# Performance work log

Measured on AMD Instinct MI355X. Metric: run time of the kernel, lower is better.

The kernel has to match this reference:

```python
import jax, jax.numpy as jnp
import numpy as np
import math

N_HEADS = 16
ROPE_THETA = 10000.0


def _rope_cos_sin(seqlen, head_dim, theta=ROPE_THETA):
    # freqs_cis = polar(1, outer(t, 1/theta^(2i/d))) -> return cos, sin parts
    inv = 1.0 / (theta ** (jnp.arange(0, head_dim, 2, dtype=jnp.float32) / head_dim))
    t = jnp.arange(seqlen, dtype=jnp.float32)
    freqs = t[:, None] * inv[None, :]          # [S, hd/2]
    return jnp.cos(freqs), jnp.sin(freqs)


def _apply_rope(x, cos, sin):
    # x: [B, S, H, hd]; treat consecutive pairs as complex, rotate by e^{i*freq}
    B, S, H, hd = x.shape
    x2 = x.astype(jnp.float32).reshape(B, S, H, hd // 2, 2)
    xr, xi = x2[..., 0], x2[..., 1]
    c = cos[None, :, None, :]
    s = sin[None, :, None, :]
    out_r = xr * c - xi * s
    out_i = xr * s + xi * c
    return jnp.stack([out_r, out_i], axis=-1).reshape(B, S, H, hd).astype(x.dtype)


def setup_inputs() -> dict:
    key = jax.random.key(0)
    ks = jax.random.split(key, 5)
    dim = 2048
    B, S = 2, 2048
    scale = 1.0 / math.sqrt(dim)
    x = jax.random.normal(ks[0], (B, S, dim), dtype=jnp.float32)
    wq = jax.random.normal(ks[1], (dim, dim), dtype=jnp.float32) * scale
    wk = jax.random.normal(ks[2], (dim, dim), dtype=jnp.float32) * scale
    wv = jax.random.normal(ks[3], (dim, dim), dtype=jnp.float32) * scale
    wo = jax.random.normal(ks[4], (dim, dim), dtype=jnp.float32) * scale
    return {"x": x, "wq": wq, "wk": wk, "wv": wv, "wo": wo}


def reference(x, wq, wk, wv, wo):
    B, S, D = x.shape
    H = N_HEADS
    hd = D // H
    # nn.Linear(bias=False): y = x @ W.T
    q = (x @ wq.T).reshape(B, S, H, hd)
    k = (x @ wk.T).reshape(B, S, H, hd)
    v = (x @ wv.T).reshape(B, S, H, hd)
    cos, sin = _rope_cos_sin(S, hd)
    q = _apply_rope(q, cos, sin)
    k = _apply_rope(k, cos, sin)
    attn = jnp.einsum('bthd,bThd->bhtT', q, k) / jnp.sqrt(jnp.float32(hd))
    attn = jax.nn.softmax(attn, axis=-1)
    out = jnp.einsum('bhtT,bThd->bthd', attn, v).reshape(B, S, D)
    return out @ wo.T
```

## Files before the change

### kernel.cpp

```cpp
#include <hip/hip_runtime.h>
#include <math.h>

typedef unsigned short u16;
typedef __bf16 bf16x8 __attribute__((ext_vector_type(8)));
typedef short s16x4 __attribute__((ext_vector_type(4)));
typedef short s16x8 __attribute__((ext_vector_type(8)));
typedef float f32x4 __attribute__((ext_vector_type(4)));

#define B_ 2
#define S_ 2048
#define D_ 2048
#define H_ 16
#define HD_ 128
#define M_ 4096
#define N3_ 6144

#define AS1(p) ((__attribute__((address_space(1))) void*)(void*)(p))
#define AS3(p) ((__attribute__((address_space(3))) void*)(p))
#define GLD16(g, l) __builtin_amdgcn_global_load_lds(AS1(g), AS3(l), 16, 0, 0)

__device__ __forceinline__ u16 f2bf(float f) {
  unsigned u = __float_as_uint(f);
  return (u16)((u + 0x7FFFu + ((u >> 16) & 1u)) >> 16);
}
__device__ __forceinline__ float bf2f(u16 v) {
  return __uint_as_float(((unsigned)v) << 16);
}

__global__ void cvt_k(const float* __restrict__ src, u16* __restrict__ dst, int n4) {
  int i = blockIdx.x * 256 + threadIdx.x;
  if (i >= n4) return;
  float4 v = ((const float4*)src)[i];
  ushort4 o;
  o.x = f2bf(v.x); o.y = f2bf(v.y); o.z = f2bf(v.z); o.w = f2bf(v.w);
  ((ushort4*)dst)[i] = o;
}

__global__ void rope_tab_k(float2* __restrict__ tab) {
  int t = blockIdx.x * 256 + threadIdx.x;
  if (t >= S_ * 64) return;
  int s = t >> 6, i = t & 63;
  double inv = exp2(-(double)i * (13.287712379549449 / 64.0));
  double fr = (double)s * inv;
  double sv, cv;
  sincos(fr, &sv, &cv);
  tab[t] = make_float2((float)cv, (float)sv);
}

template <typename OT>
__global__ __launch_bounds__(256) void gemm_bt_k(const u16* __restrict__ A,
                                                 const u16* __restrict__ B,
                                                 OT* __restrict__ C,
                                                 int M, int N, int K) {
  __shared__ alignas(16) u16 As[128 * 32];
  __shared__ alignas(16) u16 Bs[128 * 32];
  const int tid = threadIdx.x;
  const int wave = tid >> 6, lane = tid & 63;
  const int quad = lane >> 4, l16 = lane & 15;
  const int m0 = blockIdx.y * 128, n0 = blockIdx.x * 128;
  const int wm = (wave >> 1) * 64, wn = (wave & 1) * 64;
  const u16* Ag = A + (size_t)m0 * K;
  const u16* Bg = B + (size_t)n0 * K;
  f32x4 acc[4][4] = {};
  const int c0 = tid, c1 = tid + 256;
  const int r0 = c0 >> 2, k0b = (c0 & 3) * 8;
  const int r1 = c1 >> 2, k1b = (c1 & 3) * 8;
  u16* la0 = As + (size_t)(wave * 64) * 8;
  u16* la1 = As + (size_t)(256 + wave * 64) * 8;
  u16* lb0 = Bs + (size_t)(wave * 64) * 8;
  u16* lb1 = Bs + (size_t)(256 + wave * 64) * 8;
  for (int kt = 0; kt < K; kt += 32) {
    GLD16(Ag + (size_t)r0 * K + kt + k0b, la0);
    GLD16(Ag + (size_t)r1 * K + kt + k1b, la1);
    GLD16(Bg + (size_t)r0 * K + kt + k0b, lb0);
    GLD16(Bg + (size_t)r1 * K + kt + k1b, lb1);
    __syncthreads();
    bf16x8 af[4], bfr[4];
#pragma unroll
    for (int i = 0; i < 4; ++i)
      af[i] = *(const bf16x8*)&As[(wm + i * 16 + l16) * 32 + quad * 8];
#pragma unroll
    for (int j = 0; j < 4; ++j)
      bfr[j] = *(const bf16x8*)&Bs[(wn + j * 16 + l16) * 32 + quad * 8];
#pragma unroll
    for (int i = 0; i < 4; ++i)
#pragma unroll
      for (int j = 0; j < 4; ++j)
        acc[i][j] = __builtin_amdgcn_mfma_f32_16x16x32_bf16(af[i], bfr[j], acc[i][j], 0, 0, 0);
    __syncthreads();
  }
#pragma unroll
  for (int i = 0; i < 4; ++i) {
#pragma unroll
    for (int j = 0; j < 4; ++j) {
      int n = n0 + wn + j * 16 + l16;
#pragma unroll
      for (int r = 0; r < 4; ++r) {
        int m = m0 + wm + i * 16 + quad * 4 + r;
        if constexpr (sizeof(OT) == 4)
          C[(size_t)m * N + n] = acc[i][j][r];
        else
          C[(size_t)m * N + n] = f2bf(acc[i][j][r]);
      }
    }
  }
}

__global__ void rope_k(const u16* __restrict__ qkv, const float2* __restrict__ tab,
                       u16* __restrict__ Qr, u16* __restrict__ Kr) {
  int t = blockIdx.x * 256 + threadIdx.x;
  int m = t >> 10;
  int h = (t >> 6) & 15;
  int i = t & 63;
  int s = m & (S_ - 1);
  int b = m >> 11;
  float2 cs = tab[(s << 6) | i];
  const u16* qp = qkv + (size_t)m * N3_ + h * HD_ + 2 * i;
  ushort2 qv = *(const ushort2*)qp;
  ushort2 kv = *(const ushort2*)(qp + D_);
  float qr = bf2f(qv.x), qi = bf2f(qv.y);
  float kr = bf2f(kv.x), ki = bf2f(kv.y);
  ushort2 qo, ko;
  qo.x = f2bf(qr * cs.x - qi * cs.y);
  qo.y = f2bf(qr * cs.y + qi * cs.x);
  ko.x = f2bf(kr * cs.x - ki * cs.y);
  ko.y = f2bf(kr * cs.y + ki * cs.x);
  size_t o = ((size_t)(b * H_ + h) * S_ + s) * HD_ + 2 * i;
  *(ushort2*)(Qr + o) = qo;
  *(ushort2*)(Kr + o) = ko;
}

__global__ __launch_bounds__(256) void vperm_k(const u16* __restrict__ qkv,
                                               u16* __restrict__ Vp) {
  int bh = blockIdx.y;
  int b = bh >> 4, h = bh & 15;
  int t = blockIdx.x * 256 + threadIdx.x;
  int d = t & 127, g = t >> 7;
  const u16* src = qkv + ((size_t)(b * S_ + 4 * g)) * N3_ + 2 * D_ + h * HD_ + d;
  ushort4 o;
  o.x = src[0];
  o.y = src[N3_];
  o.z = src[2 * N3_];
  o.w = src[3 * N3_];
  *(ushort4*)(Vp + (size_t)bh * S_ * HD_ + (size_t)t * 4) = o;
}

#if __has_builtin(__builtin_amdgcn_mfma_f32_16x16x16bf16_1k)
#define HAS_MFMA16 1
#endif

__global__ __launch_bounds__(256, 2) void flash_k(const u16* __restrict__ Q,
                                                  const u16* __restrict__ Kc,
                                                  const u16* __restrict__ Vp,
                                                  u16* __restrict__ O) {
  __shared__ alignas(16) u16 sm[32768];
  u16* Qs = sm;
  u16* Ks = sm + 16384;
  u16* Vs = sm + 24576;
  const int tid = threadIdx.x;
  const int wave = tid >> 6, lane = tid & 63;
  const int quad = lane >> 4, l16 = lane & 15;
  const int qt = blockIdx.x, bh = blockIdx.y;
  const int b = bh >> 4, h = bh & 15;

#pragma unroll
  for (int i = 0; i < 8; ++i) {
    int c = i * 256 + tid, row = c >> 4, jl = c & 15;
    int gj = (jl & 8) | ((jl ^ row) & 7);
    GLD16(Q + ((size_t)bh * S_ + qt * 128 + row) * HD_ + gj * 8,
          Qs + (size_t)(i * 256 + wave * 64) * 8);
  }
  __syncthreads();
  bf16x8 qf[2][4];
#pragma unroll
  for (int qs = 0; qs < 2; ++qs) {
    int row = wave * 32 + qs * 16 + l16;
#pragma unroll
    for (int dk = 0; dk < 4; ++dk) {
      int c = dk * 4 + quad, pj = (c & 8) | ((c ^ row) & 7);
      qf[qs][dk] = *(const bf16x8*)&Qs[row * 128 + pj * 8];
    }
  }

  f32x4 acco[2][8] = {};
  f32x4 accl[2] = {};
  const float SCL = 0.08838834764831845f * 1.4426950408889634f;
#ifdef HAS_MFMA16
  const s16x4 ones = {(short)0x3F80, (short)0x3F80, (short)0x3F80, (short)0x3F80};
#else
  union { s16x8 s; bf16x8 b; } onesu;
  onesu.s = (s16x8){(short)0x3F80, (short)0x3F80, (short)0x3F80, (short)0x3F80,
                    (short)0x3F80, (short)0x3F80, (short)0x3F80, (short)0x3F80};
#endif

#pragma unroll 1
  for (int kt = 0; kt < 32; ++kt) {
#pragma unroll
    for (int i = 0; i < 4; ++i) {
      int c = i * 256 + tid, row = c >> 4, jl = c & 15;
      int gj = (jl & 8) | ((jl ^ row) & 7);
      GLD16(Kc + ((size_t)bh * S_ + kt * 64 + row) * HD_ + gj * 8,
            Ks + (size_t)(i * 256 + wave * 64) * 8);
    }
    const u16* vg = Vp + (size_t)bh * S_ * HD_ + (size_t)kt * 8192;
#pragma unroll
    for (int i = 0; i < 4; ++i)
      GLD16(vg + (size_t)(i * 256 + tid) * 8, Vs + (size_t)(i * 256 + wave * 64) * 8);
    __syncthreads();

    f32x4 sc[2][4] = {};
#pragma unroll
    for (int k4 = 0; k4 < 4; ++k4) {
      int row = k4 * 16 + l16;
#pragma unroll
      for (int dk = 0; dk < 4; ++dk) {
        int c = dk * 4 + quad, pj = (c & 8) | ((c ^ row) & 7);
        bf16x8 kf = *(const bf16x8*)&Ks[row * 128 + pj * 8];
        sc[0][k4] = __builtin_amdgcn_mfma_f32_16x16x32_bf16(kf, qf[0][dk], sc[0][k4], 0, 0, 0);
        sc[1][k4] = __builtin_amdgcn_mfma_f32_16x16x32_bf16(kf, qf[1][dk], sc[1][k4], 0, 0, 0);
      }
    }

#ifdef HAS_MFMA16
    s16x4 ap[2][4];
#else
    bf16x8 ap[2][4];
#endif
#pragma unroll
    for (int qs = 0; qs < 2; ++qs) {
#pragma unroll
      for (int k4 = 0; k4 < 4; ++k4) {
        f32x4 s = sc[qs][k4];
        u16 p0 = f2bf(__builtin_amdgcn_exp2f(s[0] * SCL));
        u16 p1 = f2bf(__builtin_amdgcn_exp2f(s[1] * SCL));
        u16 p2 = f2bf(__builtin_amdgcn_exp2f(s[2] * SCL));
        u16 p3 = f2bf(__builtin_amdgcn_exp2f(s[3] * SCL));
#ifdef HAS_MFMA16
        ap[qs][k4] = (s16x4){(short)p0, (short)p1, (short)p2, (short)p3};
#else
        union { s16x8 s8; bf16x8 b8; } u;
        u.s8 = (s16x8){(short)p0, (short)p1, (short)p2, (short)p3, 0, 0, 0, 0};
        ap[qs][k4] = u.b8;
#endif
      }
    }

#pragma unroll
    for (int ck = 0; ck < 4; ++ck) {
      int vbase = (ck * 4 + quad) * 512 + l16 * 4;
#pragma unroll
      for (int df = 0; df < 8; ++df) {
        s16x4 bv = *(const s16x4*)&Vs[vbase + df * 64];
#ifdef HAS_MFMA16
        acco[0][df] = __builtin_amdgcn_mfma_f32_16x16x16bf16_1k(ap[0][ck], bv, acco[0][df], 0, 0, 0);
        acco[1][df] = __builtin_amdgcn_mfma_f32_16x16x16bf16_1k(ap[1][ck], bv, acco[1][df], 0, 0, 0);
#else
        union { s16x8 s8; bf16x8 b8; } vb;
        vb.s8 = (s16x8){bv[0], bv[1], bv[2], bv[3], 0, 0, 0, 0};
        acco[0][df] = __builtin_amdgcn_mfma_f32_16x16x32_bf16(ap[0][ck], vb.b8, acco[0][df], 0, 0, 0);
        acco[1][df] = __builtin_amdgcn_mfma_f32_16x16x32_bf16(ap[1][ck], vb.b8, acco[1][df], 0, 0, 0);
#endif
      }
#ifdef HAS_MFMA16
      accl[0] = __builtin_amdgcn_mfma_f32_16x16x16bf16_1k(ones, ap[0][ck], accl[0], 0, 0, 0);
      accl[1] = __builtin_amdgcn_mfma_f32_16x16x16bf16_1k(ones, ap[1][ck], accl[1], 0, 0, 0);
#else
      accl[0] = __builtin_amdgcn_mfma_f32_16x16x32_bf16(onesu.b, ap[0][ck], accl[0], 0, 0, 0);
      accl[1] = __builtin_amdgcn_mfma_f32_16x16x32_bf16(onesu.b, ap[1][ck], accl[1], 0, 0, 0);
#endif
    }
    __syncthreads();
  }

#pragma unroll
  for (int qs = 0; qs < 2; ++qs) {
    float lv = accl[qs][0];
    float linv[4];
#pragma unroll
    for (int r = 0; r < 4; ++r) linv[r] = 1.0f / __shfl(lv, quad * 4 + r);
    int rowb = qt * 128 + wave * 32 + qs * 16 + quad * 4;
#pragma unroll
    for (int df = 0; df < 8; ++df) {
      int col = h * HD_ + df * 16 + l16;
#pragma unroll
      for (int r = 0; r < 4; ++r)
        O[((size_t)(b * S_ + rowb + r)) * D_ + col] = f2bf(acco[qs][df][r] * linv[r]);
    }
  }
}

extern "C" void kernel_launch(void* const* d_in, const int* in_sizes, int n_in,
                              void* d_out, int out_size, void* d_ws, size_t ws_size,
                              hipStream_t stream) {
  const float* x  = (const float*)d_in[0];
  const float* wq = (const float*)d_in[1];
  const float* wk = (const float*)d_in[2];
  const float* wv = (const float*)d_in[3];
  const float* wo = (const float*)d_in[4];

  size_t off = 0;
  char* ws = (char*)d_ws;
  u16* xb    = (u16*)(ws + off); off += (size_t)M_ * D_ * 2;
  u16* wqkvb = (u16*)(ws + off); off += (size_t)3 * D_ * D_ * 2;
  u16* wob   = (u16*)(ws + off); off += (size_t)D_ * D_ * 2;
  u16* qkv   = (u16*)(ws + off); off += (size_t)M_ * N3_ * 2;
  u16* Qr    = (u16*)(ws + off); off += (size_t)M_ * D_ * 2;
  u16* Kr    = (u16*)(ws + off); off += (size_t)M_ * D_ * 2;
  u16* Vp    = (u16*)(ws + off); off += (size_t)M_ * D_ * 2;
  float2* tab = (float2*)(ws + off); off += (size_t)S_ * 64 * sizeof(float2);
  u16* Ob = qkv;
  if (off > ws_size) return;

  cvt_k<<<M_ * D_ / 4 / 256, 256, 0, stream>>>(x, xb, M_ * D_ / 4);
  cvt_k<<<D_ * D_ / 4 / 256, 256, 0, stream>>>(wq, wqkvb, D_ * D_ / 4);
  cvt_k<<<D_ * D_ / 4 / 256, 256, 0, stream>>>(wk, wqkvb + (size_t)D_ * D_, D_ * D_ / 4);
  cvt_k<<<D_ * D_ / 4 / 256, 256, 0, stream>>>(wv, wqkvb + (size_t)2 * D_ * D_, D_ * D_ / 4);
  cvt_k<<<D_ * D_ / 4 / 256, 256, 0, stream>>>(wo, wob, D_ * D_ / 4);
  rope_tab_k<<<(S_ * 64) / 256, 256, 0, stream>>>(tab);
  gemm_bt_k<u16><<<dim3(N3_ / 128, M_ / 128), 256, 0, stream>>>(xb, wqkvb, qkv, M_, N3_, D_);
  rope_k<<<(M_ * H_ * 64) / 256, 256, 0, stream>>>(qkv, tab, Qr, Kr);
  vperm_k<<<dim3(S_ * HD_ / 4 / 256, B_ * H_), 256, 0, stream>>>(qkv, Vp);
  flash_k<<<dim3(S_ / 128, B_ * H_), 256, 0, stream>>>(Qr, Kr, Vp, Ob);
  gemm_bt_k<float><<<dim3(D_ / 128, M_ / 128), 256, 0, stream>>>(Ob, wob, (float*)d_out, M_, D_, D_);
}
```

Measured before the change: 439.4 us.

## Split flash attention over two KV halves with merge kernel and fuse prep kernels

The flash attention kernel now splits the key range into two halves across grid.y, doubling the block count. Each half writes unnormalized fp32 partial outputs and row sums, and a new merge kernel combines and normalizes them to bf16. Q staging now reuses a halved shared buffer so occupancy can rise to 3 blocks per CU. The conversion, rope-table, rope and V-permute kernels are fused into two launches to cut launch overhead. The cost is extra fp32 traffic for the partials and reliance on the softmax having no max subtraction, so partial sums can be added directly.

```diff
diff --git a/kernel.cpp b/kernel.cpp
--- a/kernel.cpp
+++ b/kernel.cpp
@@ -27,24 +27,42 @@
   return __uint_as_float(((unsigned)v) << 16);
 }
 
-__global__ void cvt_k(const float* __restrict__ src, u16* __restrict__ dst, int n4) {
-  int i = blockIdx.x * 256 + threadIdx.x;
-  if (i >= n4) return;
-  float4 v = ((const float4*)src)[i];
-  ushort4 o;
-  o.x = f2bf(v.x); o.y = f2bf(v.y); o.z = f2bf(v.z); o.w = f2bf(v.w);
-  ((ushort4*)dst)[i] = o;
-}
-
-__global__ void rope_tab_k(float2* __restrict__ tab) {
-  int t = blockIdx.x * 256 + threadIdx.x;
-  if (t >= S_ * 64) return;
-  int s = t >> 6, i = t & 63;
-  double inv = exp2(-(double)i * (13.287712379549449 / 64.0));
-  double fr = (double)s * inv;
-  double sv, cv;
-  sincos(fr, &sv, &cv);
-  tab[t] = make_float2((float)cv, (float)sv);
+__global__ void prep_k(const float* __restrict__ x, const float* __restrict__ wq,
+                       const float* __restrict__ wk, const float* __restrict__ wv,
+                       const float* __restrict__ wo, u16* __restrict__ xb,
+                       u16* __restrict__ wqkvb, u16* __restrict__ wob,
+                       float2* __restrict__ tab) {
+  int idx = blockIdx.x * 256 + threadIdx.x;
+  if (idx < 6291456) {
+    const float* src;
+    u16* dst;
+    if (idx < 2097152) {
+      src = x + (size_t)idx * 4;
+      dst = xb + (size_t)idx * 4;
+    } else if (idx < 5242880) {
+      int ow = idx - 2097152;
+      const float* w = ow < 1048576 ? wq : (ow < 2097152 ? wk : wv);
+      int wo_off = ow & 1048575;
+      src = w + (size_t)wo_off * 4;
+      dst = wqkvb + (size_t)ow * 4;
+    } else {
+      int ow = idx - 5242880;
+      src = wo + (size_t)ow * 4;
+      dst = wob + (size_t)ow * 4;
+    }
+    float4 v = *(const float4*)src;
+    ushort4 o;
+    o.x = f2bf(v.x); o.y = f2bf(v.y); o.z = f2bf(v.z); o.w = f2bf(v.w);
+    *(ushort4*)dst = o;
+  } else {
+    int t = idx - 6291456;
+    int s = t >> 6, i = t & 63;
+    double inv = exp2(-(double)i * (13.287712379549449 / 64.0));
+    double fr = (double)s * inv;
+    double sv, cv;
+    sincos(fr, &sv, &cv);
+    tab[t] = make_float2((float)cv, (float)sv);
+  }
 }
 
 template <typename OT>
@@ -106,80 +124,88 @@
   }
 }
 
-__global__ void rope_k(const u16* __restrict__ qkv, const float2* __restrict__ tab,
-                       u16* __restrict__ Qr, u16* __restrict__ Kr) {
-  int t = blockIdx.x * 256 + threadIdx.x;
-  int m = t >> 10;
-  int h = (t >> 6) & 15;
-  int i = t & 63;
-  int s = m & (S_ - 1);
-  int b = m >> 11;
-  float2 cs = tab[(s << 6) | i];
-  const u16* qp = qkv + (size_t)m * N3_ + h * HD_ + 2 * i;
-  ushort2 qv = *(const ushort2*)qp;
-  ushort2 kv = *(const ushort2*)(qp + D_);
-  float qr = bf2f(qv.x), qi = bf2f(qv.y);
-  float kr = bf2f(kv.x), ki = bf2f(kv.y);
-  ushort2 qo, ko;
-  qo.x = f2bf(qr * cs.x - qi * cs.y);
-  qo.y = f2bf(qr * cs.y + qi * cs.x);
-  ko.x = f2bf(kr * cs.x - ki * cs.y);
-  ko.y = f2bf(kr * cs.y + ki * cs.x);
-  size_t o = ((size_t)(b * H_ + h) * S_ + s) * HD_ + 2 * i;
-  *(ushort2*)(Qr + o) = qo;
-  *(ushort2*)(Kr + o) = ko;
-}
-
-__global__ __launch_bounds__(256) void vperm_k(const u16* __restrict__ qkv,
-                                               u16* __restrict__ Vp) {
-  int bh = blockIdx.y;
-  int b = bh >> 4, h = bh & 15;
-  int t = blockIdx.x * 256 + threadIdx.x;
-  int d = t & 127, g = t >> 7;
-  const u16* src = qkv + ((size_t)(b * S_ + 4 * g)) * N3_ + 2 * D_ + h * HD_ + d;
-  ushort4 o;
-  o.x = src[0];
-  o.y = src[N3_];
-  o.z = src[2 * N3_];
-  o.w = src[3 * N3_];
-  *(ushort4*)(Vp + (size_t)bh * S_ * HD_ + (size_t)t * 4) = o;
+__global__ void rv_k(const u16* __restrict__ qkv, const float2* __restrict__ tab,
+                     u16* __restrict__ Qr, u16* __restrict__ Kr, u16* __restrict__ Vp) {
+  int idx = blockIdx.x * 256 + threadIdx.x;
+  if (idx < 4194304) {
+    int m = idx >> 10;
+    int h = (idx >> 6) & 15;
+    int i = idx & 63;
+    int s = m & (S_ - 1);
+    int b = m >> 11;
+    float2 cs = tab[(s << 6) | i];
+    const u16* qp = qkv + (size_t)m * N3_ + h * HD_ + 2 * i;
+    ushort2 qv = *(const ushort2*)qp;
+    ushort2 kv = *(const ushort2*)(qp + D_);
+    float qr = bf2f(qv.x), qi = bf2f(qv.y);
+    float kr = bf2f(kv.x), ki = bf2f(kv.y);
+    ushort2 qo, ko;
+    qo.x = f2bf(qr * cs.x - qi * cs.y);
+    qo.y = f2bf(qr * cs.y + qi * cs.x);
+    ko.x = f2bf(kr * cs.x - ki * cs.y);
+    ko.y = f2bf(kr * cs.y + ki * cs.x);
+    size_t o = ((size_t)(b * H_ + h) * S_ + s) * HD_ + 2 * i;
+    *(ushort2*)(Qr + o) = qo;
+    *(ushort2*)(Kr + o) = ko;
+  } else {
+    int u = idx - 4194304;
+    int bh = u >> 16, t = u & 65535;
+    int b = bh >> 4, h = bh & 15;
+    int d = t & 127, g = t >> 7;
+    const u16* src = qkv + ((size_t)(b * S_ + 4 * g)) * N3_ + 2 * D_ + h * HD_ + d;
+    ushort4 o;
+    o.x = src[0];
+    o.y = src[N3_];
+    o.z = src[2 * N3_];
+    o.w = src[3 * N3_];
+    *(ushort4*)(Vp + (size_t)bh * S_ * HD_ + (size_t)t * 4) = o;
+  }
 }
 
 #if __has_builtin(__builtin_amdgcn_mfma_f32_16x16x16bf16_1k)
 #define HAS_MFMA16 1
 #endif
 
-__global__ __launch_bounds__(256, 2) void flash_k(const u16* __restrict__ Q,
+__global__ __launch_bounds__(256, 3) void flash_k(const u16* __restrict__ Q,
                                                   const u16* __restrict__ Kc,
                                                   const u16* __restrict__ Vp,
-                                                  u16* __restrict__ O) {
-  __shared__ alignas(16) u16 sm[32768];
-  u16* Qs = sm;
-  u16* Ks = sm + 16384;
-  u16* Vs = sm + 24576;
+                                                  float* __restrict__ Op0,
+                                                  float* __restrict__ Op1,
+                                                  float* __restrict__ lbuf) {
+  __shared__ alignas(16) u16 sm[16384];
+  u16* Ks = sm;
+  u16* Vs = sm + 8192;
   const int tid = threadIdx.x;
   const int wave = tid >> 6, lane = tid & 63;
   const int quad = lane >> 4, l16 = lane & 15;
-  const int qt = blockIdx.x, bh = blockIdx.y;
+  const int qt = blockIdx.x;
+  const int bh = blockIdx.y & 31, split = blockIdx.y >> 5;
   const int b = bh >> 4, h = bh & 15;
 
-#pragma unroll
-  for (int i = 0; i < 8; ++i) {
-    int c = i * 256 + tid, row = c >> 4, jl = c & 15;
-    int gj = (jl & 8) | ((jl ^ row) & 7);
-    GLD16(Q + ((size_t)bh * S_ + qt * 128 + row) * HD_ + gj * 8,
-          Qs + (size_t)(i * 256 + wave * 64) * 8);
-  }
-  __syncthreads();
   bf16x8 qf[2][4];
 #pragma unroll
-  for (int qs = 0; qs < 2; ++qs) {
-    int row = wave * 32 + qs * 16 + l16;
-#pragma unroll
-    for (int dk = 0; dk < 4; ++dk) {
-      int c = dk * 4 + quad, pj = (c & 8) | ((c ^ row) & 7);
-      qf[qs][dk] = *(const bf16x8*)&Qs[row * 128 + pj * 8];
-    }
+  for (int half = 0; half < 2; ++half) {
+#pragma unroll
+    for (int i = 0; i < 4; ++i) {
+      int c = i * 256 + tid, row = c >> 4, jl = c & 15;
+      int gj = (jl & 8) | ((jl ^ row) & 7);
+      GLD16(Q + ((size_t)bh * S_ + qt * 128 + half * 64 + row) * HD_ + gj * 8,
+            sm + (size_t)(i * 256 + wave * 64) * 8);
+    }
+    __syncthreads();
+    if ((wave >> 1) == half) {
+      int wrow = (wave & 1) * 32;
+#pragma unroll
+      for (int qs = 0; qs < 2; ++qs) {
+        int row = wrow + qs * 16 + l16;
+#pragma unroll
+        for (int dk = 0; dk < 4; ++dk) {
+          int c = dk * 4 + quad, pj = (c & 8) | ((c ^ row) & 7);
+          qf[qs][dk] = *(const bf16x8*)&sm[row * 128 + pj * 8];
+        }
+      }
+    }
+    __syncthreads();
   }
 
   f32x4 acco[2][8] = {};
@@ -193,8 +219,9 @@
                     (short)0x3F80, (short)0x3F80, (short)0x3F80, (short)0x3F80};
 #endif
 
+  const int kt0 = split * 16, kt1 = kt0 + 16;
 #pragma unroll 1
-  for (int kt = 0; kt < 32; ++kt) {
+  for (int kt = kt0; kt < kt1; ++kt) {
 #pragma unroll
     for (int i = 0; i < 4; ++i) {
       int c = i * 256 + tid, row = c >> 4, jl = c & 15;
@@ -272,21 +299,39 @@
     __syncthreads();
   }
 
+  float* op = split ? Op1 : Op0;
 #pragma unroll
   for (int qs = 0; qs < 2; ++qs) {
-    float lv = accl[qs][0];
-    float linv[4];
-#pragma unroll
-    for (int r = 0; r < 4; ++r) linv[r] = 1.0f / __shfl(lv, quad * 4 + r);
     int rowb = qt * 128 + wave * 32 + qs * 16 + quad * 4;
 #pragma unroll
     for (int df = 0; df < 8; ++df) {
       int col = h * HD_ + df * 16 + l16;
 #pragma unroll
       for (int r = 0; r < 4; ++r)
-        O[((size_t)(b * S_ + rowb + r)) * D_ + col] = f2bf(acco[qs][df][r] * linv[r]);
-    }
-  }
+        op[((size_t)(b * S_ + rowb + r)) * D_ + col] = acco[qs][df][r];
+    }
+    if (quad == 0)
+      lbuf[(size_t)split * 65536 + bh * 2048 + qt * 128 + wave * 32 + qs * 16 + l16] =
+          accl[qs][0];
+  }
+}
+
+__global__ void merge_k(const float* __restrict__ Op0, const float* __restrict__ Op1,
+                        const float* __restrict__ lbuf, u16* __restrict__ Ob) {
+  int i4 = blockIdx.x * 256 + threadIdx.x;
+  int row = i4 >> 9, col4 = i4 & 511;
+  int b = row >> 11, s = row & 2047, h4 = col4 >> 5;
+  int bh = (b << 4) | h4;
+  float l = lbuf[bh * 2048 + s] + lbuf[65536 + bh * 2048 + s];
+  float inv = 1.0f / l;
+  float4 a = ((const float4*)Op0)[i4];
+  float4 c = ((const float4*)Op1)[i4];
+  ushort4 o;
+  o.x = f2bf((a.x + c.x) * inv);
+  o.y = f2bf((a.y + c.y) * inv);
+  o.z = f2bf((a.z + c.z) * inv);
+  o.w = f2bf((a.w + c.w) * inv);
+  ((ushort4*)Ob)[i4] = o;
 }
 
 extern "C" void kernel_launch(void* const* d_in, const int* in_sizes, int n_in,
@@ -308,18 +353,16 @@
   u16* Kr    = (u16*)(ws + off); off += (size_t)M_ * D_ * 2;
   u16* Vp    = (u16*)(ws + off); off += (size_t)M_ * D_ * 2;
   float2* tab = (float2*)(ws + off); off += (size_t)S_ * 64 * sizeof(float2);
-  u16* Ob = qkv;
+  float* Op0  = (float*)ws;
+  u16*   Ob   = qkv;
+  float* Op1  = (float*)(ws + ((size_t)64 << 20));
+  float* lbuf = (float*)tab;
   if (off > ws_size) return;
 
-  cvt_k<<<M_ * D_ / 4 / 256, 256, 0, stream>>>(x, xb, M_ * D_ / 4);
-  cvt_k<<<D_ * D_ / 4 / 256, 256, 0, stream>>>(wq, wqkvb, D_ * D_ / 4);
-  cvt_k<<<D_ * D_ / 4 / 256, 256, 0, stream>>>(wk, wqkvb + (size_t)D_ * D_, D_ * D_ / 4);
-  cvt_k<<<D_ * D_ / 4 / 256, 256, 0, stream>>>(wv, wqkvb + (size_t)2 * D_ * D_, D_ * D_ / 4);
-  cvt_k<<<D_ * D_ / 4 / 256, 256, 0, stream>>>(wo, wob, D_ * D_ / 4);
-  rope_tab_k<<<(S_ * 64) / 256, 256, 0, stream>>>(tab);
+  prep_k<<<25088, 256, 0, stream>>>(x, wq, wk, wv, wo, xb, wqkvb, wob, tab);
   gemm_bt_k<u16><<<dim3(N3_ / 128, M_ / 128), 256, 0, stream>>>(xb, wqkvb, qkv, M_, N3_, D_);
-  rope_k<<<(M_ * H_ * 64) / 256, 256, 0, stream>>>(qkv, tab, Qr, Kr);
-  vperm_k<<<dim3(S_ * HD_ / 4 / 256, B_ * H_), 256, 0, stream>>>(qkv, Vp);
-  flash_k<<<dim3(S_ / 128, B_ * H_), 256, 0, stream>>>(Qr, Kr, Vp, Ob);
+  rv_k<<<24576, 256, 0, stream>>>(qkv, tab, Qr, Kr, Vp);
+  flash_k<<<dim3(S_ / 128, 64), 256, 0, stream>>>(Qr, Kr, Vp, Op0, Op1, lbuf);
+  merge_k<<<(M_ * D_ / 4) / 256, 256, 0, stream>>>(Op0, Op1, lbuf, Ob);
   gemm_bt_k<float><<<dim3(D_ / 128, M_ / 128), 256, 0, stream>>>(Ob, wob, (float*)d_out, M_, D_, D_);
 }
```

After: 462.7 us. +5.3%, slower.
